# Kernel tuning notes

Measured on AMD Instinct MI355X. Metric: run time of the kernel, lower is better.

## Reference

```python
import jax, jax.numpy as jnp
import numpy as np

N = 50000       # nodes
E = 800000      # edges (avg degree 16)
H = 64          # hidden_channels
T = 4           # towers
F = H // T      # per-tower channels (divide_input=True) = 16
NAGG, NSC = 5, 3
# degree histogram passed as mol_deg -> avg log-degree scaler constant (as in PyG PNAConv)
MOL_DEG = np.array([0, 5, 15, 30, 25, 15, 7, 2, 1], dtype=np.float64)
_bins = np.arange(len(MOL_DEG))
AVG_LOG = float((np.log(_bins + 1.0) * MOL_DEG).sum() / MOL_DEG.sum())


def setup_inputs() -> dict:
    key = jax.random.key(0)
    ks = jax.random.split(key, 12)
    g = lambda k, shp, s=0.1: jax.random.normal(k, shp, dtype=jnp.float32) * s
    return {
        "atom_x": g(ks[0], (N, H), 1.0),
        "bond_emb": g(ks[1], (5, H)),                      # Embedding(5, H)
        "edge_w": g(ks[2], (H, F)), "edge_b": jnp.zeros((F,), jnp.float32),
        "pre_w1": g(ks[3], (T, 3 * F, F)), "pre_b1": jnp.zeros((T, F), jnp.float32),
        "pre_w2": g(ks[4], (T, F, F)), "pre_b2": jnp.zeros((T, F), jnp.float32),
        "post_w1": g(ks[5], (T, (1 + NAGG * NSC) * F, F)), "post_b1": jnp.zeros((T, F), jnp.float32),
        "post_w2": g(ks[6], (T, F, F)), "post_b2": jnp.zeros((T, F), jnp.float32),
        "lin_w": g(ks[7], (H, H)), "lin_b": jnp.zeros((H,), jnp.float32),
        "ln_g": jnp.ones((H,), jnp.float32), "ln_b": jnp.zeros((H,), jnp.float32),
        "bond_x": jax.random.randint(ks[8], (E,), 0, 5),
        "atom_edge_index": jax.random.randint(ks[9], (2, E), 0, N),
    }


def reference(atom_x, bond_emb, edge_w, edge_b, pre_w1, pre_b1, pre_w2, pre_b2,
              post_w1, post_b1, post_w2, post_b2, lin_w, lin_b, ln_g, ln_b,
              bond_x, atom_edge_index):
    src, dst = atom_edge_index[0], atom_edge_index[1]
    # bond encoder + PNA edge encoder (edge_dim -> F_in)
    e = bond_emb[bond_x] @ edge_w + edge_b                       # [E, F]
    xt = atom_x.reshape(N, T, F)                                 # divide_input
    x_j, x_i = xt[src], xt[dst]                                  # [E, T, F]
    et = jnp.broadcast_to(e[:, None, :], (E, T, F))
    h = jnp.concatenate([x_i, x_j, et], axis=-1)                 # [E, T, 3F]
    # per-tower pre-MLP (Linear -> ReLU -> Linear)
    h = jax.nn.relu(jnp.einsum('etf,tfg->etg', h, pre_w1) + pre_b1)
    h = jnp.einsum('etf,tfg->etg', h, pre_w2) + pre_b2           # messages [E, T, F]

    s = jax.ops.segment_sum(h, dst, num_segments=N)
    cnt = jax.ops.segment_sum(jnp.ones((E,), h.dtype), dst, num_segments=N)
    cnt_c = jnp.maximum(cnt, 1.0)[:, None, None]
    mean = s / cnt_c
    mean2 = jax.ops.segment_sum(h * h, dst, num_segments=N) / cnt_c
    std = jnp.sqrt(jax.nn.relu(mean2 - mean * mean) + 1e-5)
    has = (cnt > 0)[:, None, None]
    mn = jnp.where(has, jax.ops.segment_min(h, dst, num_segments=N), 0.0)
    mx = jnp.where(has, jax.ops.segment_max(h, dst, num_segments=N), 0.0)
    agg = jnp.concatenate([s, mean, mn, mx, std], axis=-1)       # [N, T, 5F]

    # degree scalers (deg clamped to 1, as in PyG DegreeScalerAggregation)
    ld = jnp.log(jnp.maximum(cnt, 1.0) + 1.0)[:, None, None]
    agg = jnp.concatenate([agg, agg * (ld / AVG_LOG), agg * (AVG_LOG / ld)], axis=-1)  # [N, T, 15F]

    out = jnp.concatenate([xt, agg], axis=-1)                    # [N, T, 16F]
    # per-tower post-MLP, then mix towers with final Linear
    out = jax.nn.relu(jnp.einsum('ntf,tfg->ntg', out, post_w1) + post_b1)
    out = jnp.einsum('ntf,tfg->ntg', out, post_w2) + post_b2     # [N, T, F]
    out = out.reshape(N, H) @ lin_w + lin_b                      # [N, H]

    # LayerNorm + ReLU + residual (dropout is identity in eval)
    mu = out.mean(-1, keepdims=True)
    var = out.var(-1, keepdims=True)
    ln = (out - mu) / jnp.sqrt(var + 1e-5) * ln_g + ln_b
    return atom_x + jax.nn.relu(ln)
```

## Files before the change

kernel.cpp:

```cpp
#include <hip/hip_runtime.h>
#include <cstdint>

typedef unsigned short u16;

#define AVG_LOG_F 1.4862356961977451f
#define MAXD 64

#define OFF_W2   3072
#define OFF_PW1  4096
#define OFF_PW2  20480
#define OFF_LW   21504
#define OFF_PB1  25600
#define OFF_PB2  25664
#define OFF_QB1  25728
#define OFF_QB2  25792
#define OFF_LB   25856
#define OFF_LG   25920
#define OFF_LBN  25984
#define OFF_EWT  26128
#define IB       26448

__device__ __forceinline__ float bf2f(u16 u) {
    return __uint_as_float(((unsigned)u) << 16);
}
__device__ __forceinline__ u16 f2bf(float f) {
    unsigned u = __float_as_uint(f);
    u += 0x7fffu + ((u >> 16) & 1u);
    return (u16)(u >> 16);
}
__device__ __forceinline__ float rdin(const void* p, long j, int mode) {
    if (mode == 0) return bf2f(((const u16*)p)[j]);
    return ((const float*)p)[j];
}
template <int MODE>
__device__ __forceinline__ void load16c(const void* p, long base, float* o) {
    if (MODE == 0) {
        const u16* q = (const u16*)p + base;
        uint4 a = *(const uint4*)q;
        uint4 b = *(const uint4*)(q + 8);
        o[0]  = __uint_as_float(a.x << 16); o[1]  = __uint_as_float(a.x & 0xffff0000u);
        o[2]  = __uint_as_float(a.y << 16); o[3]  = __uint_as_float(a.y & 0xffff0000u);
        o[4]  = __uint_as_float(a.z << 16); o[5]  = __uint_as_float(a.z & 0xffff0000u);
        o[6]  = __uint_as_float(a.w << 16); o[7]  = __uint_as_float(a.w & 0xffff0000u);
        o[8]  = __uint_as_float(b.x << 16); o[9]  = __uint_as_float(b.x & 0xffff0000u);
        o[10] = __uint_as_float(b.y << 16); o[11] = __uint_as_float(b.y & 0xffff0000u);
        o[12] = __uint_as_float(b.z << 16); o[13] = __uint_as_float(b.z & 0xffff0000u);
        o[14] = __uint_as_float(b.w << 16); o[15] = __uint_as_float(b.w & 0xffff0000u);
    } else {
        const float* q = (const float*)p + base;
        float4 a = *(const float4*)q;
        float4 b = *(const float4*)(q + 4);
        float4 c = *(const float4*)(q + 8);
        float4 d = *(const float4*)(q + 12);
        o[0]=a.x; o[1]=a.y; o[2]=a.z; o[3]=a.w;
        o[4]=b.x; o[5]=b.y; o[6]=b.z; o[7]=b.w;
        o[8]=c.x; o[9]=c.y; o[10]=c.z; o[11]=c.w;
        o[12]=d.x; o[13]=d.y; o[14]=d.z; o[15]=d.w;
    }
}

template <int MODE>
__device__ __forceinline__ void y_loop(const void* ax, const void* pre_w1, float* wsY, float* wsXW,
                                       int Nn, int wave, int nwaves, int l) {
    const int t = l >> 4, g = l & 15;
    float wxi[16], wxj[16];
#pragma unroll
    for (int f = 0; f < 16; f++) {
        wxi[f] = rdin(pre_w1, t * 768 + f * 16 + g, MODE);
        wxj[f] = rdin(pre_w1, t * 768 + (16 + f) * 16 + g, MODE);
    }
    for (int n = wave; n < Nn; n += nwaves) {
        float xj[16];
        load16c<MODE>(ax, (long)n * 64 + t * 16, xj);
        float accY = 0.f, accX = 0.f;
#pragma unroll
        for (int f = 0; f < 16; f++) {
            accY = fmaf(xj[f], wxj[f], accY);
            accX = fmaf(xj[f], wxi[f], accX);
        }
        wsY[(long)n * 64 + l]  = accY;
        wsXW[(long)n * 64 + l] = accX;
    }
}

__global__ __launch_bounds__(256) void k_prep(
    const int* __restrict__ dstp, const int* __restrict__ srcp, const int* __restrict__ bondp,
    const void* bond_emb, const void* edge_w, const void* edge_b,
    const void* pre_w1, const void* pre_b1, const void* pre_w2, const void* pre_b2,
    const void* post_w1, const void* post_b1, const void* post_w2, const void* post_b2,
    const void* lin_w, const void* lin_b, const void* ln_g, const void* ln_b,
    const void* ax, float* wsf, float* wsY, float* wsXW,
    int* __restrict__ cnt, int* __restrict__ pk, int* modep,
    int Nn, int E, int NIB)
{
    int tid = threadIdx.x;
    if ((int)blockIdx.x >= NIB) {
        int e = ((int)blockIdx.x - NIB) * 256 + tid;
        if (e < E) {
            int d = dstp[e];
            int pos = atomicAdd(&cnt[d], 1);
            if (pos < MAXD) pk[d * MAXD + pos] = (srcp[e] << 9) | (bondp[e] & 7);
        }
        return;
    }
    __shared__ int csh;
    __shared__ float ET[80];
    if (tid == 0) csh = 0;
    __syncthreads();
    {
        unsigned v = ((const unsigned*)ax)[tid];
        unsigned lo = v & 0xffffu;
        int ee = (int)((lo >> 7) & 0xff);
        int isbf = (lo == 0u) || (ee >= 110 && ee <= 140);
        atomicAdd(&csh, isbf);
    }
    __syncthreads();
    int mode = (csh >= 192) ? 0 : 1;

    int b = (int)blockIdx.x;
    int gt = b * 256 + tid;
    int gs = NIB * 256;
    if (b == 0 && tid == 0) modep[0] = mode;

    for (int j = gt; j < 1024; j += gs)  wsf[OFF_W2 + j]  = rdin(pre_w2, j, mode);
    for (int j = gt; j < 16384; j += gs) wsf[OFF_PW1 + j] = rdin(post_w1, j, mode);
    for (int j = gt; j < 1024; j += gs)  wsf[OFF_PW2 + j] = rdin(post_w2, j, mode);
    for (int j = gt; j < 4096; j += gs)  wsf[OFF_LW + j]  = rdin(lin_w, j, mode);
    for (int j = gt; j < 64; j += gs) {
        wsf[OFF_PB1 + j] = rdin(pre_b1, j, mode);
        wsf[OFF_PB2 + j] = rdin(pre_b2, j, mode);
        wsf[OFF_QB1 + j] = rdin(post_b1, j, mode);
        wsf[OFF_QB2 + j] = rdin(post_b2, j, mode);
        wsf[OFF_LB + j]  = rdin(lin_b, j, mode);
        wsf[OFF_LG + j]  = rdin(ln_g, j, mode);
        wsf[OFF_LBN + j] = rdin(ln_b, j, mode);
    }
    if (b == 0) {
        if (tid < 80) {
            int bb = tid >> 4, f = tid & 15;
            float acc = rdin(edge_b, f, mode);
            for (int k = 0; k < 64; k++)
                acc = fmaf(rdin(bond_emb, bb * 64 + k, mode), rdin(edge_w, k * 16 + f, mode), acc);
            ET[tid] = acc;
        }
        __syncthreads();
        for (int j = tid; j < 320; j += 256) {
            int bb = j >> 6, ll = j & 63, tt = ll >> 4, gg = ll & 15;
            float acc = rdin(pre_b1, tt * 16 + gg, mode);
#pragma unroll
            for (int f = 0; f < 16; f++)
                acc = fmaf(ET[bb * 16 + f], rdin(pre_w1, tt * 768 + (32 + f) * 16 + gg, mode), acc);
            wsf[OFF_EWT + j] = acc;
        }
    }
    int wave = gt >> 6;
    int nwaves = gs >> 6;
    int l = tid & 63;
    if (mode == 0) y_loop<0>(ax, pre_w1, wsY, wsXW, Nn, wave, nwaves, l);
    else           y_loop<1>(ax, pre_w1, wsY, wsXW, Nn, wave, nwaves, l);
}

__global__ __launch_bounds__(256, 6) void k_node(
    const void* __restrict__ ax, const float* __restrict__ Yp, const float* __restrict__ XWp,
    const int* __restrict__ pk, const int* __restrict__ cnt,
    const float* __restrict__ wsf, void* __restrict__ outp,
    const int* __restrict__ modep, int Nn)
{
    __shared__ float hb[4][16][64];
    __shared__ float zws[4][5][64];
    __shared__ float qp[4][4][64];
    __shared__ float xrow[4][64];
    __shared__ float scl1s[4], scl2s[4];
    const int w = threadIdx.x >> 6;
    const int l = threadIdx.x & 63;
    const int t = l >> 4;
    const int g = l & 15;
    const int n = blockIdx.x * 4 + w;
    const int mode = modep[0];
    const bool active = (n < Nn);
    const int nn = active ? n : 0;

    const float* W2  = wsf + OFF_W2  + t * 256;
    const float* PW1 = wsf + OFF_PW1 + t * 4096;
    const float* PW2 = wsf + OFF_PW2 + t * 256;

    float w2c[16];
#pragma unroll
    for (int f = 0; f < 16; f++) w2c[f] = W2[f * 16 + g];
    float pb2g = wsf[OFF_PB2 + t * 16 + g];
    float qb1g = wsf[OFF_QB1 + t * 16 + g];
    float qb2g = wsf[OFF_QB2 + t * 16 + g];

    int deg = active ? cnt[nn] : 0;
    if (deg > MAXD) deg = MAXD;

    int   pkvAll = pk[nn * MAXD + l];
    float XWv    = XWp[(long)nn * 64 + l];
    zws[w][0][l] = XWv + wsf[OFF_EWT + 0 * 64 + l];
    zws[w][1][l] = XWv + wsf[OFF_EWT + 1 * 64 + l];
    zws[w][2][l] = XWv + wsf[OFF_EWT + 2 * 64 + l];
    zws[w][3][l] = XWv + wsf[OFF_EWT + 3 * 64 + l];
    zws[w][4][l] = XWv + wsf[OFF_EWT + 4 * 64 + l];
    xrow[w][l]   = rdin(ax, (long)nn * 64 + l, mode);

    float s = 0.f, s2 = 0.f, mn = 3.0e38f, mx = -3.0e38f;

    auto phaseA = [&](int srclane, int k) {
        int v = __builtin_amdgcn_readlane(pkvAll, srclane);
        float yv = Yp[(v >> 3) + l];
        float zt = zws[w][v & 7][l];
        hb[w][k][l] = fmaxf(yv + zt, 0.f);
    };
    auto phaseB = [&](int k) {
        const float4* hp = (const float4*)&hb[w][k][t * 16];
        float4 h0 = hp[0], h1 = hp[1], h2 = hp[2], h3 = hp[3];
        float m = pb2g;
        m = fmaf(h0.x, w2c[0],  m); m = fmaf(h0.y, w2c[1],  m);
        m = fmaf(h0.z, w2c[2],  m); m = fmaf(h0.w, w2c[3],  m);
        m = fmaf(h1.x, w2c[4],  m); m = fmaf(h1.y, w2c[5],  m);
        m = fmaf(h1.z, w2c[6],  m); m = fmaf(h1.w, w2c[7],  m);
        m = fmaf(h2.x, w2c[8],  m); m = fmaf(h2.y, w2c[9],  m);
        m = fmaf(h2.z, w2c[10], m); m = fmaf(h2.w, w2c[11], m);
        m = fmaf(h3.x, w2c[12], m); m = fmaf(h3.y, w2c[13], m);
        m = fmaf(h3.z, w2c[14], m); m = fmaf(h3.w, w2c[15], m);
        s += m;
        s2 = fmaf(m, m, s2);
        mn = fminf(mn, m);
        mx = fmaxf(mx, m);
    };

#pragma unroll
    for (int kb = 0; kb < MAXD; kb += 16) {
        if (kb >= deg) break;
        int B = deg - kb; if (B > 16) B = 16;
        if (B == 16) {
#pragma unroll
            for (int k = 0; k < 16; k++) phaseA(kb + k, k);
#pragma unroll 4
            for (int k = 0; k < 16; k++) phaseB(k);
        } else {
            for (int k = 0; k < B; k++) phaseA(kb + k, k);
            for (int k = 0; k < B; k++) phaseB(k);
        }
    }

    if (deg == 0) { mn = 0.f; mx = 0.f; }
    float cf = (float)(deg > 0 ? deg : 1);
    float inv = 1.0f / cf;
    float mean = s * inv;
    float var = s2 * inv - mean * mean;
    float sd = sqrtf(fmaxf(var, 0.f) + 1e-5f);
    float ldv = logf(cf + 1.0f);
    float sc1 = ldv * (1.0f / AVG_LOG_F);
    float sc2 = AVG_LOG_F / ldv;

    hb[w][0][l] = s;
    hb[w][1][l] = mean;
    hb[w][2][l] = mn;
    hb[w][3][l] = mx;
    hb[w][4][l] = sd;
    if (l == 0) { scl1s[w] = sc1; scl2s[w] = sc2; }
    __syncthreads();

    const int F0 = w * 4;
    float q0[4] = {0,0,0,0}, q1[4] = {0,0,0,0}, q2[4] = {0,0,0,0};
    {
        float xa[4][4];
#pragma unroll
        for (int nd = 0; nd < 4; nd++) {
            float4 v = *(const float4*)&xrow[nd][t * 16 + F0];
            xa[nd][0] = v.x; xa[nd][1] = v.y; xa[nd][2] = v.z; xa[nd][3] = v.w;
        }
#pragma unroll
        for (int fi = 0; fi < 4; fi++) {
            float wv = PW1[(F0 + fi) * 16 + g];
#pragma unroll
            for (int nd = 0; nd < 4; nd++) q0[nd] = fmaf(xa[nd][fi], wv, q0[nd]);
        }
    }
#pragma unroll
    for (int a = 0; a < 5; a++) {
        float xa[4][4];
#pragma unroll
        for (int nd = 0; nd < 4; nd++) {
            float4 v = *(const float4*)&hb[nd][a][t * 16 + F0];
            xa[nd][0] = v.x; xa[nd][1] = v.y; xa[nd][2] = v.z; xa[nd][3] = v.w;
        }
        const int rb = 16 + a * 16;
#pragma unroll
        for (int fi = 0; fi < 4; fi++) {
            const int r = (rb + F0 + fi) * 16 + g;
            float w0  = PW1[r];
            float w1  = PW1[r + 80 * 16];
            float w2v = PW1[r + 160 * 16];
#pragma unroll
            for (int nd = 0; nd < 4; nd++) {
                float x = xa[nd][fi];
                q0[nd] = fmaf(x, w0,  q0[nd]);
                q1[nd] = fmaf(x, w1,  q1[nd]);
                q2[nd] = fmaf(x, w2v, q2[nd]);
            }
        }
    }
#pragma unroll
    for (int nd = 0; nd < 4; nd++)
        qp[w][nd][l] = fmaf(scl2s[nd], q2[nd], fmaf(scl1s[nd], q1[nd], q0[nd]));
    __syncthreads();

    {
        float q0s = qp[0][w][l] + qp[1][w][l] + qp[2][w][l] + qp[3][w][l];
        float p1 = fmaxf(q0s + qb1g, 0.f);
        hb[w][5][l] = p1;
        float pw2c[16];
#pragma unroll
        for (int f = 0; f < 16; f++) pw2c[f] = PW2[f * 16 + g];
        float m2 = qb2g;
        const float4* pp = (const float4*)&hb[w][5][t * 16];
        float4 p0 = pp[0], r1 = pp[1], r2 = pp[2], r3 = pp[3];
        m2 = fmaf(p0.x, pw2c[0],  m2); m2 = fmaf(p0.y, pw2c[1],  m2);
        m2 = fmaf(p0.z, pw2c[2],  m2); m2 = fmaf(p0.w, pw2c[3],  m2);
        m2 = fmaf(r1.x, pw2c[4],  m2); m2 = fmaf(r1.y, pw2c[5],  m2);
        m2 = fmaf(r1.z, pw2c[6],  m2); m2 = fmaf(r1.w, pw2c[7],  m2);
        m2 = fmaf(r2.x, pw2c[8],  m2); m2 = fmaf(r2.y, pw2c[9],  m2);
        m2 = fmaf(r2.z, pw2c[10], m2); m2 = fmaf(r2.w, pw2c[11], m2);
        m2 = fmaf(r3.x, pw2c[12], m2); m2 = fmaf(r3.y, pw2c[13], m2);
        m2 = fmaf(r3.z, pw2c[14], m2); m2 = fmaf(r3.w, pw2c[15], m2);
        hb[w][6][l] = m2;
    }
    __syncthreads();

    {
        const float* LW = wsf + OFF_LW;
        const int fb = w * 16;
        float lw[4] = {0,0,0,0};
#pragma unroll
        for (int c = 0; c < 4; c++) {
            float pa[4][4];
#pragma unroll
            for (int nd = 0; nd < 4; nd++) {
                float4 v = *(const float4*)&hb[nd][6][fb + 4 * c];
                pa[nd][0] = v.x; pa[nd][1] = v.y; pa[nd][2] = v.z; pa[nd][3] = v.w;
            }
#pragma unroll
            for (int fi = 0; fi < 4; fi++) {
                float wl = LW[(fb + 4 * c + fi) * 64 + l];
#pragma unroll
                for (int nd = 0; nd < 4; nd++) lw[nd] = fmaf(pa[nd][fi], wl, lw[nd]);
            }
        }
#pragma unroll
        for (int nd = 0; nd < 4; nd++) qp[w][nd][l] = lw[nd];
    }
    __syncthreads();

    {
        float a = wsf[OFF_LB + l] + qp[0][w][l] + qp[1][w][l] + qp[2][w][l] + qp[3][w][l];
        float s1 = a, sq = a * a;
#pragma unroll
        for (int o = 1; o < 64; o <<= 1) { s1 += __shfl_xor(s1, o); sq += __shfl_xor(sq, o); }
        float mu = s1 * (1.0f / 64.0f);
        float varl = sq * (1.0f / 64.0f) - mu * mu;
        float ln = (a - mu) * rsqrtf(varl + 1e-5f) * wsf[OFF_LG + l] + wsf[OFF_LBN + l];
        if (active) {
            long idx = (long)n * 64 + l;
            float res = xrow[w][l] + fmaxf(ln, 0.f);
            if (mode == 0) ((u16*)outp)[idx] = f2bf(res);
            else           ((float*)outp)[idx] = res;
        }
    }
}

extern "C" void kernel_launch(void* const* d_in, const int* in_sizes, int n_in,
                              void* d_out, int out_size, void* d_ws, size_t ws_size,
                              hipStream_t stream) {
    const void* atom_x   = d_in[0];
    const void* bond_emb = d_in[1];
    const void* edge_w   = d_in[2];
    const void* edge_b   = d_in[3];
    const void* pre_w1   = d_in[4];
    const void* pre_b1   = d_in[5];
    const void* pre_w2   = d_in[6];
    const void* pre_b2   = d_in[7];
    const void* post_w1  = d_in[8];
    const void* post_b1  = d_in[9];
    const void* post_w2  = d_in[10];
    const void* post_b2  = d_in[11];
    const void* lin_w    = d_in[12];
    const void* lin_b    = d_in[13];
    const void* ln_g     = d_in[14];
    const void* ln_b     = d_in[15];
    const int* bond_x    = (const int*)d_in[16];
    const int* aei       = (const int*)d_in[17];

    int E  = in_sizes[16];
    int Nn = in_sizes[0] / 64;
    const int* srcp = aei;
    const int* dstp = aei + E;

    float* wsf = (float*)d_ws;
    int*   wsi = (int*)d_ws;

    size_t o = IB;
    int* modep = wsi + o; o += 16;
    int* cnt   = wsi + o; o += Nn;
    o = (o + 63) & ~(size_t)63;
    int* pk    = wsi + o; o += (size_t)Nn * MAXD;
    float* Yp  = (float*)(wsi + o); o += (size_t)Nn * 64;
    float* XWp = (float*)(wsi + o); o += (size_t)Nn * 64;

    const int NIB  = 1600;
    const int SBLK = (E + 255) / 256;

    (void)hipMemsetAsync(cnt, 0, (size_t)Nn * sizeof(int), stream);
    k_prep<<<NIB + SBLK, 256, 0, stream>>>(dstp, srcp, bond_x,
                                           bond_emb, edge_w, edge_b,
                                           pre_w1, pre_b1, pre_w2, pre_b2,
                                           post_w1, post_b1, post_w2, post_b2,
                                           lin_w, lin_b, ln_g, ln_b,
                                           atom_x, wsf, Yp, XWp, cnt, pk, modep, Nn, E, NIB);
    dim3 gn((Nn + 3) / 4, 1, 1);
    k_node<<<gn, 256, 0, stream>>>(atom_x, Yp, XWp, pk, cnt, wsf, d_out, modep, Nn);
}
```

Before: 308.0 us.

## Compute per-edge 16x16 tower matvec with DPP row rotations instead of LDS

Replaces the LDS staging of per-edge hidden vectors (write to hb, then float4 reads) with in-register cross-lane exchange using DPP row_ror within 16-lane rows, with the weights pre-rotated per lane. A runtime probe detects the rotation direction so the weight indexing matches. The edge loop now batches 8 gathers ahead of compute. The hb buffer shrinks and the occupancy hint drops from 6 to 4, trading LDS traffic and barriers for extra VALU DPP ops and possibly fewer resident waves.

```diff
diff --git a/kernel.cpp b/kernel.cpp
--- a/kernel.cpp
+++ b/kernel.cpp
@@ -160,13 +160,13 @@
     else           y_loop<1>(ax, pre_w1, wsY, wsXW, Nn, wave, nwaves, l);
 }
 
-__global__ __launch_bounds__(256, 6) void k_node(
+__global__ __launch_bounds__(256, 4) void k_node(
     const void* __restrict__ ax, const float* __restrict__ Yp, const float* __restrict__ XWp,
     const int* __restrict__ pk, const int* __restrict__ cnt,
     const float* __restrict__ wsf, void* __restrict__ outp,
     const int* __restrict__ modep, int Nn)
 {
-    __shared__ float hb[4][16][64];
+    __shared__ float hb[4][8][64];
     __shared__ float zws[4][5][64];
     __shared__ float qp[4][4][64];
     __shared__ float xrow[4][64];
@@ -184,9 +184,14 @@
     const float* PW1 = wsf + OFF_PW1 + t * 4096;
     const float* PW2 = wsf + OFF_PW2 + t * 256;
 
-    float w2c[16];
-#pragma unroll
-    for (int f = 0; f < 16; f++) w2c[f] = W2[f * 16 + g];
+    int probe = __builtin_amdgcn_update_dpp(0, l & 15, 0x121, 0xf, 0xf, false);
+    int p0 = __builtin_amdgcn_readfirstlane(probe);
+    const int dir = (p0 == 1) ? 1 : -1;
+
+    float w2r[16];
+#pragma unroll
+    for (int r = 0; r < 16; r++) w2r[r] = W2[((g + dir * r) & 15) * 16 + g];
+
     float pb2g = wsf[OFF_PB2 + t * 16 + g];
     float qb1g = wsf[OFF_QB1 + t * 16 + g];
     float qb2g = wsf[OFF_QB2 + t * 16 + g];
@@ -205,44 +210,45 @@
 
     float s = 0.f, s2 = 0.f, mn = 3.0e38f, mx = -3.0e38f;
 
-    auto phaseA = [&](int srclane, int k) {
-        int v = __builtin_amdgcn_readlane(pkvAll, srclane);
-        float yv = Yp[(v >> 3) + l];
-        float zt = zws[w][v & 7][l];
-        hb[w][k][l] = fmaxf(yv + zt, 0.f);
-    };
-    auto phaseB = [&](int k) {
-        const float4* hp = (const float4*)&hb[w][k][t * 16];
-        float4 h0 = hp[0], h1 = hp[1], h2 = hp[2], h3 = hp[3];
-        float m = pb2g;
-        m = fmaf(h0.x, w2c[0],  m); m = fmaf(h0.y, w2c[1],  m);
-        m = fmaf(h0.z, w2c[2],  m); m = fmaf(h0.w, w2c[3],  m);
-        m = fmaf(h1.x, w2c[4],  m); m = fmaf(h1.y, w2c[5],  m);
-        m = fmaf(h1.z, w2c[6],  m); m = fmaf(h1.w, w2c[7],  m);
-        m = fmaf(h2.x, w2c[8],  m); m = fmaf(h2.y, w2c[9],  m);
-        m = fmaf(h2.z, w2c[10], m); m = fmaf(h2.w, w2c[11], m);
-        m = fmaf(h3.x, w2c[12], m); m = fmaf(h3.y, w2c[13], m);
-        m = fmaf(h3.z, w2c[14], m); m = fmaf(h3.w, w2c[15], m);
-        s += m;
-        s2 = fmaf(m, m, s2);
-        mn = fminf(mn, m);
-        mx = fmaxf(mx, m);
-    };
-
-#pragma unroll
-    for (int kb = 0; kb < MAXD; kb += 16) {
-        if (kb >= deg) break;
-        int B = deg - kb; if (B > 16) B = 16;
-        if (B == 16) {
-#pragma unroll
-            for (int k = 0; k < 16; k++) phaseA(kb + k, k);
-#pragma unroll 4
-            for (int k = 0; k < 16; k++) phaseB(k);
-        } else {
-            for (int k = 0; k < B; k++) phaseA(kb + k, k);
-            for (int k = 0; k < B; k++) phaseB(k);
-        }
-    }
+#define ROTFMA(r, ctrl)                                                              \
+    {                                                                                \
+        int tmp_ = __builtin_amdgcn_update_dpp(0, hi, ctrl, 0xf, 0xf, false);        \
+        float hv_ = __int_as_float(tmp_);                                            \
+        if ((r) & 1) mb = fmaf(hv_, w2r[r], mb);                                     \
+        else         ma = fmaf(hv_, w2r[r], ma);                                     \
+    }
+
+    for (int kb = 0; kb < deg; kb += 8) {
+        float yv[8];
+        int   vs[8];
+#pragma unroll
+        for (int k = 0; k < 8; k++) {
+            if (kb + k < deg) {
+                vs[k] = __builtin_amdgcn_readlane(pkvAll, kb + k);
+                yv[k] = Yp[(vs[k] >> 3) + l];
+            }
+        }
+#pragma unroll
+        for (int k = 0; k < 8; k++) {
+            if (kb + k < deg) {
+                float h = fmaxf(yv[k] + zws[w][vs[k] & 7][l], 0.f);
+                int hi = __float_as_uint(h);
+                float ma = fmaf(h, w2r[0], pb2g);
+                float mb = 0.f;
+                ROTFMA(1, 0x121);  ROTFMA(2, 0x122);  ROTFMA(3, 0x123);
+                ROTFMA(4, 0x124);  ROTFMA(5, 0x125);  ROTFMA(6, 0x126);
+                ROTFMA(7, 0x127);  ROTFMA(8, 0x128);  ROTFMA(9, 0x129);
+                ROTFMA(10, 0x12A); ROTFMA(11, 0x12B); ROTFMA(12, 0x12C);
+                ROTFMA(13, 0x12D); ROTFMA(14, 0x12E); ROTFMA(15, 0x12F);
+                float m = ma + mb;
+                s += m;
+                s2 = fmaf(m, m, s2);
+                mn = fminf(mn, m);
+                mx = fmaxf(mx, m);
+            }
+        }
+    }
+#undef ROTFMA
 
     if (deg == 0) { mn = 0.f; mx = 0.f; }
     float cf = (float)(deg > 0 ? deg : 1);
@@ -316,9 +322,9 @@
         for (int f = 0; f < 16; f++) pw2c[f] = PW2[f * 16 + g];
         float m2 = qb2g;
         const float4* pp = (const float4*)&hb[w][5][t * 16];
-        float4 p0 = pp[0], r1 = pp[1], r2 = pp[2], r3 = pp[3];
-        m2 = fmaf(p0.x, pw2c[0],  m2); m2 = fmaf(p0.y, pw2c[1],  m2);
-        m2 = fmaf(p0.z, pw2c[2],  m2); m2 = fmaf(p0.w, pw2c[3],  m2);
+        float4 p0v = pp[0], r1 = pp[1], r2 = pp[2], r3 = pp[3];
+        m2 = fmaf(p0v.x, pw2c[0],  m2); m2 = fmaf(p0v.y, pw2c[1],  m2);
+        m2 = fmaf(p0v.z, pw2c[2],  m2); m2 = fmaf(p0v.w, pw2c[3],  m2);
         m2 = fmaf(r1.x, pw2c[4],  m2); m2 = fmaf(r1.y, pw2c[5],  m2);
         m2 = fmaf(r1.z, pw2c[6],  m2); m2 = fmaf(r1.w, pw2c[7],  m2);
         m2 = fmaf(r2.x, pw2c[8],  m2); m2 = fmaf(r2.y, pw2c[9],  m2);
```

Result: faster. 298.9 us (-3.0%).
